# Performance work log

Measured on AMD Instinct MI355X. Metric: run time of the kernel, lower is better.

Reference implementation:

```python
import jax, jax.numpy as jnp
import numpy as np

SEG_NUM = 100000
D_SEG = 128
D_S = 258       # 2*D_SEG + 2 (offset)
D_M7 = 512
D_M8 = 256
MASK = 64
T_SLOTS = 96
B = 4096
CAND_OUT = 4            # candidate_layer out_features
DW_COLS = D_M8 - CAND_OUT  # 252
BN_EPS = 1e-6
COS_EPS = 1e-8


def setup_inputs() -> dict:
    key = jax.random.key(0)
    ks = jax.random.split(key, 20)
    s = 0.02
    return {
        "src": jax.random.randint(ks[0], (B,), 0, SEG_NUM),
        "dest": jax.random.randint(ks[1], (B,), 0, SEG_NUM),
        "t": jax.random.randint(ks[2], (B,), 0, T_SLOTS),
        "candidates": jax.random.randint(ks[3], (B, MASK), 0, SEG_NUM),
        "offset": jax.random.normal(ks[4], (B, 4), jnp.float32),
        "emb_feat": jax.random.normal(ks[5], (SEG_NUM, D_SEG), jnp.float32) * s,
        "emb_dest": jax.random.normal(ks[6], (SEG_NUM, D_SEG), jnp.float32) * s,
        "w1": jax.random.normal(ks[7], (D_M7, D_S), jnp.float32) * s,
        "b1": jnp.zeros((D_M7,), jnp.float32),
        "bn_gamma": jnp.ones((D_M7,), jnp.float32),
        "bn_beta": jnp.zeros((D_M7,), jnp.float32),
        "bn_mean": jax.random.normal(ks[8], (D_M7,), jnp.float32) * s,
        "bn_var": jax.random.uniform(ks[9], (D_M7,), jnp.float32, 0.5, 1.5),
        "w2": jax.random.normal(ks[10], (D_M8, D_M7), jnp.float32) * s,
        "b2": jnp.zeros((D_M8,), jnp.float32),
        "dense_w": jax.random.normal(ks[11], (SEG_NUM, DW_COLS), jnp.float32) * s,
        "dense_b": jnp.zeros((SEG_NUM,), jnp.float32),
        "cand_w": jax.random.normal(ks[12], (CAND_OUT, 2), jnp.float32) * s,
        "cand_b": jnp.zeros((CAND_OUT,), jnp.float32),
        "segs_src": jax.random.normal(ks[13], (SEG_NUM, 2), jnp.float32),
        "segs_trg": jax.random.normal(ks[14], (SEG_NUM, 2), jnp.float32),
        "traffic_pop": jax.random.uniform(ks[15], (SEG_NUM, T_SLOTS), jnp.float32),
    }


def reference(src, dest, t, candidates, offset, emb_feat, emb_dest, w1, b1,
              bn_gamma, bn_beta, bn_mean, bn_var, w2, b2, dense_w, dense_b,
              cand_w, cand_b, segs_src, segs_trg, traffic_pop):
    # --- ODEncoder: embedding gathers + offset features ---
    code = jnp.concatenate([emb_feat[src], emb_dest[dest], offset[:, 1:3]], axis=1)  # [B, 258]
    # --- MLP: Linear -> BatchNorm1d (eval, running stats) -> ReLU -> Linear ---
    h = code @ w1.T + b1
    h = (h - bn_mean) * (bn_gamma / jnp.sqrt(bn_var + BN_EPS)) + bn_beta
    h = jax.nn.relu(h)
    out = h @ w2.T + b2  # [B, 256]
    # --- gather dense rows by candidate index ---
    sub_w = dense_w[candidates]   # [B, M, 252]
    sub_b = dense_b[candidates]   # [B, M]
    # --- traffic feature: traffic_pop[candidate, t] ---
    traffic_feat = traffic_pop[candidates, t[:, None]]  # [B, M]
    # --- cosine similarity between dest-direction and segment direction ---
    v1 = segs_src[dest][:, None, :] - segs_src[candidates]  # [B, M, 2]
    v2 = segs_trg[candidates] - segs_src[candidates]        # [B, M, 2]
    num = jnp.sum(v1 * v2, axis=-1)
    den = jnp.maximum(jnp.linalg.norm(v1, axis=-1) * jnp.linalg.norm(v2, axis=-1), COS_EPS)
    cos_feat = num / den  # [B, M]
    cand_feat = jnp.stack([cos_feat, traffic_feat], axis=-1)  # [B, M, 2]
    emb_cand = cand_feat @ cand_w.T + cand_b                  # [B, M, 4]
    W = jnp.concatenate([sub_w, emb_cand], axis=-1)           # [B, M, 256]
    # --- batched small matvec + bias ---
    logits = jnp.einsum('bmd,bd->bm', W, out) + sub_b         # [B, M]
    return logits
```

## Files before the change

kernel.cpp:

```cpp
#include <hip/hip_runtime.h>


#define BATCH 4096
#define DSEG 128
#define DS_ 258
#define DM7 512
#define DM8 256
#define NCAND 64
#define DWC 252
#define TSLOTS 96
#define SEGN 100000
#define MLP_BLOCKS 256
#define CONV_BLOCKS 768

typedef short bf16x8 __attribute__((ext_vector_type(8)));
typedef short bf16x4 __attribute__((ext_vector_type(4)));
typedef float f32x4 __attribute__((ext_vector_type(4)));

static __device__ __forceinline__ short f2bf(float f) {
    union { float f; unsigned u; } v; v.f = f;
    unsigned r = (v.u + 0x7FFFu + ((v.u >> 16) & 1u)) >> 16;
    return (short)r;
}
static __device__ __forceinline__ bf16x4 cvt4(float4 v) {
    bf16x4 s;
    s[0] = f2bf(v.x); s[1] = f2bf(v.y); s[2] = f2bf(v.z); s[3] = f2bf(v.w);
    return s;
}
static __device__ __forceinline__ float bfu2f(unsigned u16) {
    union { unsigned u; float f; } v; v.u = u16 << 16; return v.f;
}

template <bool CONV>
__global__ __launch_bounds__(512) void fused_kernel(
    const int* __restrict__ src, const int* __restrict__ dest,
    const float* __restrict__ offset,
    const float* __restrict__ emb_feat, const float* __restrict__ emb_dest,
    const float* __restrict__ w1, const float* __restrict__ b1,
    const float* __restrict__ bn_gamma, const float* __restrict__ bn_beta,
    const float* __restrict__ bn_mean, const float* __restrict__ bn_var,
    const float* __restrict__ w2, const float* __restrict__ b2,
    const float* __restrict__ dense_w, short* __restrict__ wtab,
    float* __restrict__ out_ws)
{
    __shared__ __align__(16) short hlds[16][520];
    const int tid = threadIdx.x;

    if (CONV && blockIdx.x >= MLP_BLOCKS) {
        const size_t T = (size_t)CONV_BLOCKS * 512;
        const size_t n4 = (size_t)SEGN * DWC / 4;
        const float4* __restrict__ s4 = (const float4*)dense_w;
        bf16x4* __restrict__ d4 = (bf16x4*)wtab;
        for (size_t i = (size_t)(blockIdx.x - MLP_BLOCKS) * 512 + tid; i < n4; i += T) {
            d4[i] = cvt4(s4[i]);
        }
        return;
    }

    const int w    = tid >> 6;
    const int lane = tid & 63;
    const int lg   = lane >> 4;
    const int lr   = lane & 15;
    const int b0   = blockIdx.x * 16;

    const int si = src[b0 + lr];
    const int di = dest[b0 + lr];
    const float* fb = emb_feat + (size_t)si * DSEG;
    const float* db = emb_dest + (size_t)di * DSEG;
    bf16x8 a1[8];
#pragma unroll
    for (int s = 0; s < 8; ++s) {
        const float* p = (s < 4) ? (fb + s * 32 + lg * 8)
                                 : (db + (s - 4) * 32 + lg * 8);
        const float4 x = *(const float4*)p;
        const float4 y = *(const float4*)(p + 4);
        bf16x8 t;
        t[0] = f2bf(x.x); t[1] = f2bf(x.y); t[2] = f2bf(x.z); t[3] = f2bf(x.w);
        t[4] = f2bf(y.x); t[5] = f2bf(y.y); t[6] = f2bf(y.z); t[7] = f2bf(y.w);
        a1[s] = t;
    }
    float off1[4], off2[4];
#pragma unroll
    for (int q = 0; q < 4; ++q) {
        const float4 o = *(const float4*)(offset + (size_t)(b0 + lg * 4 + q) * 4);
        off1[q] = o.y; off2[q] = o.z;
    }

#pragma unroll
    for (int nt = 0; nt < 4; ++nt) {
        const int n = (w * 4 + nt) * 16 + lr;
        const float* wrow = w1 + (size_t)n * DS_;
        f32x4 acc = {0.f, 0.f, 0.f, 0.f};
#pragma unroll
        for (int s = 0; s < 8; ++s) {
            const float* p = wrow + s * 32 + lg * 8;
            const float2 x0 = *(const float2*)(p);
            const float2 x1 = *(const float2*)(p + 2);
            const float2 x2 = *(const float2*)(p + 4);
            const float2 x3 = *(const float2*)(p + 6);
            bf16x8 bb;
            bb[0] = f2bf(x0.x); bb[1] = f2bf(x0.y); bb[2] = f2bf(x1.x); bb[3] = f2bf(x1.y);
            bb[4] = f2bf(x2.x); bb[5] = f2bf(x2.y); bb[6] = f2bf(x3.x); bb[7] = f2bf(x3.y);
            acc = __builtin_amdgcn_mfma_f32_16x16x32_bf16(a1[s], bb, acc, 0, 0, 0);
        }
        const float2 wtail = *(const float2*)(wrow + 256);
        const float scale = bn_gamma[n] / sqrtf(bn_var[n] + 1e-6f);
        const float shift = bn_beta[n] - bn_mean[n] * scale;
        const float bias  = b1[n];
#pragma unroll
        for (int q = 0; q < 4; ++q) {
            float v = acc[q] + bias + off1[q] * wtail.x + off2[q] * wtail.y;
            v = fmaf(v, scale, shift);
            v = fmaxf(v, 0.f);
            hlds[lg * 4 + q][n] = f2bf(v);
        }
    }
    __syncthreads();

    bf16x8 a2[16];
#pragma unroll
    for (int s = 0; s < 16; ++s) {
        a2[s] = *(const bf16x8*)&hlds[lr][s * 32 + lg * 8];
    }
#pragma unroll
    for (int nt = 0; nt < 2; ++nt) {
        const int n = (w * 2 + nt) * 16 + lr;
        const float* wrow = w2 + (size_t)n * DM7;
        f32x4 acc = {0.f, 0.f, 0.f, 0.f};
#pragma unroll
        for (int s = 0; s < 16; ++s) {
            const float4 x = *(const float4*)(wrow + s * 32 + lg * 8);
            const float4 y = *(const float4*)(wrow + s * 32 + lg * 8 + 4);
            bf16x8 bb;
            bb[0] = f2bf(x.x); bb[1] = f2bf(x.y); bb[2] = f2bf(x.z); bb[3] = f2bf(x.w);
            bb[4] = f2bf(y.x); bb[5] = f2bf(y.y); bb[6] = f2bf(y.z); bb[7] = f2bf(y.w);
            acc = __builtin_amdgcn_mfma_f32_16x16x32_bf16(a2[s], bb, acc, 0, 0, 0);
        }
        const float bias = b2[n];
#pragma unroll
        for (int q = 0; q < 4; ++q) {
            out_ws[(size_t)(b0 + lg * 4 + q) * DM8 + n] = acc[q] + bias;
        }
    }
}

template <bool BF16TAB>
__global__ __launch_bounds__(256) void logits_kernel_t(
    const int* __restrict__ dest, const int* __restrict__ tt,
    const int* __restrict__ candidates,
    const float* __restrict__ dense_w, const unsigned short* __restrict__ wtab,
    const float* __restrict__ dense_b,
    const float* __restrict__ cand_w, const float* __restrict__ cand_b,
    const float* __restrict__ segs_src, const float* __restrict__ segs_trg,
    const float* __restrict__ traffic_pop,
    const float* __restrict__ out_ws,
    float* __restrict__ logits)
{
    __shared__ float plds[4][16][67];
    const int b = blockIdx.x;
    const int tid = threadIdx.x;
    const int wave = tid >> 6;
    const int lane = tid & 63;
    const int mbase = wave * 16;

    int candv = 0;
    if (lane < 16) candv = candidates[b * NCAND + mbase + lane];

    const int ll = (lane < 63) ? lane : 62;
    float4 dwf[16];
    uint2  dwb[16];
    if (BF16TAB) {
#pragma unroll
        for (int i = 0; i < 16; ++i) {
            const int ci = __shfl(candv, i, 64);
            dwb[i] = *(const uint2*)(wtab + (size_t)ci * DWC + ll * 4);
        }
    } else {
#pragma unroll
        for (int i = 0; i < 16; ++i) {
            const int ci = __shfl(candv, i, 64);
            dwf[i] = *(const float4*)(dense_w + (size_t)ci * DWC + ll * 4);
        }
    }

    float4 o4 = *(const float4*)(out_ws + (size_t)b * DM8 + ll * 4);
    if (lane == 63) { o4.x = 0.f; o4.y = 0.f; o4.z = 0.f; o4.w = 0.f; }

    float tail = 0.f;
    if (lane < 16) {
        const float4 t4 = *(const float4*)(out_ws + (size_t)b * DM8 + DWC);
        const int db = dest[b];
        const float2 dsx = *(const float2*)(segs_src + 2 * (size_t)db);
        const float2 sx = *(const float2*)(segs_src + 2 * (size_t)candv);
        const float2 tx = *(const float2*)(segs_trg + 2 * (size_t)candv);
        const float v1x = dsx.x - sx.x, v1y = dsx.y - sx.y;
        const float v2x = tx.x - sx.x, v2y = tx.y - sx.y;
        const float num = v1x * v2x + v1y * v2y;
        const float den = fmaxf(sqrtf(v1x * v1x + v1y * v1y) *
                                sqrtf(v2x * v2x + v2y * v2y), 1e-8f);
        const float cosv = num / den;
        const float tf = traffic_pop[(size_t)candv * TSLOTS + tt[b]];
        const float e0 = fmaf(cosv, cand_w[0], fmaf(tf, cand_w[1], cand_b[0]));
        const float e1 = fmaf(cosv, cand_w[2], fmaf(tf, cand_w[3], cand_b[1]));
        const float e2 = fmaf(cosv, cand_w[4], fmaf(tf, cand_w[5], cand_b[2]));
        const float e3 = fmaf(cosv, cand_w[6], fmaf(tf, cand_w[7], cand_b[3]));
        tail = e0 * t4.x + e1 * t4.y + e2 * t4.z + e3 * t4.w + dense_b[candv];
    }

#pragma unroll
    for (int i = 0; i < 16; ++i) {
        float p;
        if (BF16TAB) {
            p =      bfu2f(dwb[i].x & 0xFFFFu) * o4.x;
            p = fmaf(bfu2f(dwb[i].x >> 16),      o4.y, p);
            p = fmaf(bfu2f(dwb[i].y & 0xFFFFu),  o4.z, p);
            p = fmaf(bfu2f(dwb[i].y >> 16),      o4.w, p);
        } else {
            p = dwf[i].x * o4.x + dwf[i].y * o4.y + dwf[i].z * o4.z + dwf[i].w * o4.w;
        }
        plds[wave][i][lane] = p;
    }
    __syncthreads();

    const int cc = lane >> 2;
    const int qq = lane & 3;
    float s = 0.f;
#pragma unroll
    for (int j = 0; j < 16; ++j) s += plds[wave][cc][qq * 16 + j];
    s += __shfl_xor(s, 1, 64);
    s += __shfl_xor(s, 2, 64);
    const float tl = __shfl(tail, cc, 64);
    if (qq == 0) logits[(size_t)b * NCAND + mbase + cc] = s + tl;
}

extern "C" void kernel_launch(void* const* d_in, const int* in_sizes, int n_in,
                              void* d_out, int out_size, void* d_ws, size_t ws_size,
                              hipStream_t stream) {
    const int*   src         = (const int*)d_in[0];
    const int*   dest        = (const int*)d_in[1];
    const int*   tt          = (const int*)d_in[2];
    const int*   candidates  = (const int*)d_in[3];
    const float* offset      = (const float*)d_in[4];
    const float* emb_feat    = (const float*)d_in[5];
    const float* emb_dest    = (const float*)d_in[6];
    const float* w1          = (const float*)d_in[7];
    const float* b1          = (const float*)d_in[8];
    const float* bn_gamma    = (const float*)d_in[9];
    const float* bn_beta     = (const float*)d_in[10];
    const float* bn_mean     = (const float*)d_in[11];
    const float* bn_var      = (const float*)d_in[12];
    const float* w2          = (const float*)d_in[13];
    const float* b2          = (const float*)d_in[14];
    const float* dense_w     = (const float*)d_in[15];
    const float* dense_b     = (const float*)d_in[16];
    const float* cand_w      = (const float*)d_in[17];
    const float* cand_b      = (const float*)d_in[18];
    const float* segs_src    = (const float*)d_in[19];
    const float* segs_trg    = (const float*)d_in[20];
    const float* traffic_pop = (const float*)d_in[21];

    float* out_ws = (float*)d_ws;
    const size_t OUT_WS_BYTES = (size_t)BATCH * DM8 * 4;
    const size_t WTAB_BYTES   = (size_t)SEGN * DWC * 2;
    short* wtab = (short*)((char*)d_ws + OUT_WS_BYTES);
    const bool use_tab = ws_size >= OUT_WS_BYTES + WTAB_BYTES;
    float* logits = (float*)d_out;

    if (use_tab) {
        fused_kernel<true><<<MLP_BLOCKS + CONV_BLOCKS, 512, 0, stream>>>(
            src, dest, offset, emb_feat, emb_dest,
            w1, b1, bn_gamma, bn_beta, bn_mean, bn_var, w2, b2,
            dense_w, wtab, out_ws);
        logits_kernel_t<true><<<BATCH, 256, 0, stream>>>(
            dest, tt, candidates, dense_w, (const unsigned short*)wtab, dense_b,
            cand_w, cand_b, segs_src, segs_trg, traffic_pop, out_ws, logits);
    } else {
        fused_kernel<false><<<MLP_BLOCKS, 512, 0, stream>>>(
            src, dest, offset, emb_feat, emb_dest,
            w1, b1, bn_gamma, bn_beta, bn_mean, bn_var, w2, b2,
            dense_w, wtab, out_ws);
        logits_kernel_t<false><<<BATCH, 256, 0, stream>>>(
            dest, tt, candidates, dense_w, (const unsigned short*)wtab, dense_b,
            cand_w, cand_b, segs_src, segs_trg, traffic_pop, out_ws, logits);
    }
}
```

Baseline: 86.06 us.

## Split conversion into its own kernel and process 32 rows per MLP block

The dense_w fp32-to-bf16 table conversion moves out of the fused launch into a standalone kernel. Each thread now converts 16 floats per iteration, across 2048 blocks of 256 threads, to keep more loads in flight. The MLP kernel now handles 32 batch rows per block with two MFMA accumulators, so each converted w1/w2 weight fragment is reused twice and weight traffic is halved. The cost is that the MLP no longer runs alongside the memory-bound conversion, and registers per thread go up.

```diff
diff --git a/kernel.cpp b/kernel.cpp
--- a/kernel.cpp
+++ b/kernel.cpp
@@ -10,8 +10,8 @@
 #define DWC 252
 #define TSLOTS 96
 #define SEGN 100000
-#define MLP_BLOCKS 256
-#define CONV_BLOCKS 768
+#define CONV_BLOCKS 2048
+#define MLP_ROWS 32
 
 typedef short bf16x8 __attribute__((ext_vector_type(8)));
 typedef short bf16x4 __attribute__((ext_vector_type(4)));
@@ -22,17 +22,34 @@
     unsigned r = (v.u + 0x7FFFu + ((v.u >> 16) & 1u)) >> 16;
     return (short)r;
 }
-static __device__ __forceinline__ bf16x4 cvt4(float4 v) {
-    bf16x4 s;
-    s[0] = f2bf(v.x); s[1] = f2bf(v.y); s[2] = f2bf(v.z); s[3] = f2bf(v.w);
+static __device__ __forceinline__ bf16x8 pack8(float4 a, float4 b) {
+    bf16x8 s;
+    s[0] = f2bf(a.x); s[1] = f2bf(a.y); s[2] = f2bf(a.z); s[3] = f2bf(a.w);
+    s[4] = f2bf(b.x); s[5] = f2bf(b.y); s[6] = f2bf(b.z); s[7] = f2bf(b.w);
     return s;
 }
 static __device__ __forceinline__ float bfu2f(unsigned u16) {
     union { unsigned u; float f; } v; v.u = u16 << 16; return v.f;
 }
 
-template <bool CONV>
-__global__ __launch_bounds__(512) void fused_kernel(
+__global__ __launch_bounds__(256) void conv_kernel(
+    const float* __restrict__ dense_w, short* __restrict__ wtab)
+{
+    const size_t T = (size_t)CONV_BLOCKS * 256;
+    const size_t n16 = (size_t)SEGN * DWC / 16;
+    const float4* __restrict__ s4 = (const float4*)dense_w;
+    bf16x8* __restrict__ d8 = (bf16x8*)wtab;
+    for (size_t c = (size_t)blockIdx.x * 256 + threadIdx.x; c < n16; c += T) {
+        const float4 v0 = s4[4 * c];
+        const float4 v1 = s4[4 * c + 1];
+        const float4 v2 = s4[4 * c + 2];
+        const float4 v3 = s4[4 * c + 3];
+        d8[2 * c]     = pack8(v0, v1);
+        d8[2 * c + 1] = pack8(v2, v3);
+    }
+}
+
+__global__ __launch_bounds__(512) void mlp_kernel(
     const int* __restrict__ src, const int* __restrict__ dest,
     const float* __restrict__ offset,
     const float* __restrict__ emb_feat, const float* __restrict__ emb_dest,
@@ -40,57 +57,46 @@
     const float* __restrict__ bn_gamma, const float* __restrict__ bn_beta,
     const float* __restrict__ bn_mean, const float* __restrict__ bn_var,
     const float* __restrict__ w2, const float* __restrict__ b2,
-    const float* __restrict__ dense_w, short* __restrict__ wtab,
     float* __restrict__ out_ws)
 {
-    __shared__ __align__(16) short hlds[16][520];
+    __shared__ __align__(16) short hlds[MLP_ROWS][520];
     const int tid = threadIdx.x;
-
-    if (CONV && blockIdx.x >= MLP_BLOCKS) {
-        const size_t T = (size_t)CONV_BLOCKS * 512;
-        const size_t n4 = (size_t)SEGN * DWC / 4;
-        const float4* __restrict__ s4 = (const float4*)dense_w;
-        bf16x4* __restrict__ d4 = (bf16x4*)wtab;
-        for (size_t i = (size_t)(blockIdx.x - MLP_BLOCKS) * 512 + tid; i < n4; i += T) {
-            d4[i] = cvt4(s4[i]);
-        }
-        return;
-    }
-
     const int w    = tid >> 6;
     const int lane = tid & 63;
     const int lg   = lane >> 4;
     const int lr   = lane & 15;
-    const int b0   = blockIdx.x * 16;
-
-    const int si = src[b0 + lr];
-    const int di = dest[b0 + lr];
-    const float* fb = emb_feat + (size_t)si * DSEG;
-    const float* db = emb_dest + (size_t)di * DSEG;
-    bf16x8 a1[8];
-#pragma unroll
-    for (int s = 0; s < 8; ++s) {
-        const float* p = (s < 4) ? (fb + s * 32 + lg * 8)
-                                 : (db + (s - 4) * 32 + lg * 8);
-        const float4 x = *(const float4*)p;
-        const float4 y = *(const float4*)(p + 4);
-        bf16x8 t;
-        t[0] = f2bf(x.x); t[1] = f2bf(x.y); t[2] = f2bf(x.z); t[3] = f2bf(x.w);
-        t[4] = f2bf(y.x); t[5] = f2bf(y.y); t[6] = f2bf(y.z); t[7] = f2bf(y.w);
-        a1[s] = t;
-    }
-    float off1[4], off2[4];
-#pragma unroll
-    for (int q = 0; q < 4; ++q) {
-        const float4 o = *(const float4*)(offset + (size_t)(b0 + lg * 4 + q) * 4);
-        off1[q] = o.y; off2[q] = o.z;
-    }
+    const int b0   = blockIdx.x * MLP_ROWS;
+
+    bf16x8 a1[2][8];
+#pragma unroll
+    for (int mt = 0; mt < 2; ++mt) {
+        const int row = b0 + mt * 16 + lr;
+        const float* fb = emb_feat + (size_t)src[row] * DSEG;
+        const float* db = emb_dest + (size_t)dest[row] * DSEG;
+#pragma unroll
+        for (int s = 0; s < 8; ++s) {
+            const float* p = (s < 4) ? (fb + s * 32 + lg * 8)
+                                     : (db + (s - 4) * 32 + lg * 8);
+            const float4 x = *(const float4*)p;
+            const float4 y = *(const float4*)(p + 4);
+            a1[mt][s] = pack8(x, y);
+        }
+    }
+    float off1[2][4], off2[2][4];
+#pragma unroll
+    for (int mt = 0; mt < 2; ++mt)
+#pragma unroll
+        for (int q = 0; q < 4; ++q) {
+            const float4 o = *(const float4*)(offset + (size_t)(b0 + mt * 16 + lg * 4 + q) * 4);
+            off1[mt][q] = o.y; off2[mt][q] = o.z;
+        }
 
 #pragma unroll
     for (int nt = 0; nt < 4; ++nt) {
         const int n = (w * 4 + nt) * 16 + lr;
         const float* wrow = w1 + (size_t)n * DS_;
-        f32x4 acc = {0.f, 0.f, 0.f, 0.f};
+        f32x4 acc0 = {0.f, 0.f, 0.f, 0.f};
+        f32x4 acc1 = {0.f, 0.f, 0.f, 0.f};
 #pragma unroll
         for (int s = 0; s < 8; ++s) {
             const float* p = wrow + s * 32 + lg * 8;
@@ -101,7 +107,8 @@
             bf16x8 bb;
             bb[0] = f2bf(x0.x); bb[1] = f2bf(x0.y); bb[2] = f2bf(x1.x); bb[3] = f2bf(x1.y);
             bb[4] = f2bf(x2.x); bb[5] = f2bf(x2.y); bb[6] = f2bf(x3.x); bb[7] = f2bf(x3.y);
-            acc = __builtin_amdgcn_mfma_f32_16x16x32_bf16(a1[s], bb, acc, 0, 0, 0);
+            acc0 = __builtin_amdgcn_mfma_f32_16x16x32_bf16(a1[0][s], bb, acc0, 0, 0, 0);
+            acc1 = __builtin_amdgcn_mfma_f32_16x16x32_bf16(a1[1][s], bb, acc1, 0, 0, 0);
         }
         const float2 wtail = *(const float2*)(wrow + 256);
         const float scale = bn_gamma[n] / sqrtf(bn_var[n] + 1e-6f);
@@ -109,37 +116,37 @@
         const float bias  = b1[n];
 #pragma unroll
         for (int q = 0; q < 4; ++q) {
-            float v = acc[q] + bias + off1[q] * wtail.x + off2[q] * wtail.y;
-            v = fmaf(v, scale, shift);
-            v = fmaxf(v, 0.f);
-            hlds[lg * 4 + q][n] = f2bf(v);
+            float v0 = acc0[q] + bias + off1[0][q] * wtail.x + off2[0][q] * wtail.y;
+            v0 = fmaxf(fmaf(v0, scale, shift), 0.f);
+            hlds[lg * 4 + q][n] = f2bf(v0);
+            float v1 = acc1[q] + bias + off1[1][q] * wtail.x + off2[1][q] * wtail.y;
+            v1 = fmaxf(fmaf(v1, scale, shift), 0.f);
+            hlds[16 + lg * 4 + q][n] = f2bf(v1);
         }
     }
     __syncthreads();
 
-    bf16x8 a2[16];
-#pragma unroll
-    for (int s = 0; s < 16; ++s) {
-        a2[s] = *(const bf16x8*)&hlds[lr][s * 32 + lg * 8];
-    }
 #pragma unroll
     for (int nt = 0; nt < 2; ++nt) {
         const int n = (w * 2 + nt) * 16 + lr;
         const float* wrow = w2 + (size_t)n * DM7;
-        f32x4 acc = {0.f, 0.f, 0.f, 0.f};
+        f32x4 acc0 = {0.f, 0.f, 0.f, 0.f};
+        f32x4 acc1 = {0.f, 0.f, 0.f, 0.f};
 #pragma unroll
         for (int s = 0; s < 16; ++s) {
             const float4 x = *(const float4*)(wrow + s * 32 + lg * 8);
             const float4 y = *(const float4*)(wrow + s * 32 + lg * 8 + 4);
-            bf16x8 bb;
-            bb[0] = f2bf(x.x); bb[1] = f2bf(x.y); bb[2] = f2bf(x.z); bb[3] = f2bf(x.w);
-            bb[4] = f2bf(y.x); bb[5] = f2bf(y.y); bb[6] = f2bf(y.z); bb[7] = f2bf(y.w);
-            acc = __builtin_amdgcn_mfma_f32_16x16x32_bf16(a2[s], bb, acc, 0, 0, 0);
+            const bf16x8 bb = pack8(x, y);
+            const bf16x8 aa0 = *(const bf16x8*)&hlds[lr][s * 32 + lg * 8];
+            const bf16x8 aa1 = *(const bf16x8*)&hlds[16 + lr][s * 32 + lg * 8];
+            acc0 = __builtin_amdgcn_mfma_f32_16x16x32_bf16(aa0, bb, acc0, 0, 0, 0);
+            acc1 = __builtin_amdgcn_mfma_f32_16x16x32_bf16(aa1, bb, acc1, 0, 0, 0);
         }
         const float bias = b2[n];
 #pragma unroll
         for (int q = 0; q < 4; ++q) {
-            out_ws[(size_t)(b0 + lg * 4 + q) * DM8 + n] = acc[q] + bias;
+            out_ws[(size_t)(b0 + lg * 4 + q) * DM8 + n] = acc0[q] + bias;
+            out_ws[(size_t)(b0 + 16 + lg * 4 + q) * DM8 + n] = acc1[q] + bias;
         }
     }
 }
@@ -267,18 +274,16 @@
     float* logits = (float*)d_out;
 
     if (use_tab) {
-        fused_kernel<true><<<MLP_BLOCKS + CONV_BLOCKS, 512, 0, stream>>>(
-            src, dest, offset, emb_feat, emb_dest,
-            w1, b1, bn_gamma, bn_beta, bn_mean, bn_var, w2, b2,
-            dense_w, wtab, out_ws);
+        conv_kernel<<<CONV_BLOCKS, 256, 0, stream>>>(dense_w, wtab);
+    }
+    mlp_kernel<<<BATCH / MLP_ROWS, 512, 0, stream>>>(
+        src, dest, offset, emb_feat, emb_dest,
+        w1, b1, bn_gamma, bn_beta, bn_mean, bn_var, w2, b2, out_ws);
+    if (use_tab) {
         logits_kernel_t<true><<<BATCH, 256, 0, stream>>>(
             dest, tt, candidates, dense_w, (const unsigned short*)wtab, dense_b,
             cand_w, cand_b, segs_src, segs_trg, traffic_pop, out_ws, logits);
     } else {
-        fused_kernel<false><<<MLP_BLOCKS, 512, 0, stream>>>(
-            src, dest, offset, emb_feat, emb_dest,
-            w1, b1, bn_gamma, bn_beta, bn_mean, bn_var, w2, b2,
-            dense_w, wtab, out_ws);
         logits_kernel_t<false><<<BATCH, 256, 0, stream>>>(
             dest, tt, candidates, dense_w, (const unsigned short*)wtab, dense_b,
             cand_w, cand_b, segs_src, segs_trg, traffic_pop, out_ws, logits);
```

Result: slower. 95.89 us (+11.4%).
